# Optimization experiments

Hardware: AMD Instinct MI355X
Metric: run time of the kernel (lower is better)

Reference implementation:

```python
import jax, jax.numpy as jnp
import numpy as np

B, T, E, H, W = 2, 1024, 1024, 8, 31
D = 2 * W + 1  # head dim must equal 2*window_size+1 for the rel-pos broadcast


def _ln(x, w, b):
    mu = jnp.mean(x, axis=-1, keepdims=True)
    var = jnp.mean(jnp.square(x - mu), axis=-1, keepdims=True)
    return (x - mu) * jax.lax.rsqrt(var + 1e-5) * w + b


def setup_inputs() -> dict:
    key = jax.random.key(0)
    k = jax.random.split(key, 8)
    s = 0.02
    return {
        "x": jax.random.normal(k[0], (B, T, E // 2), jnp.float32),
        "ln1_w": jnp.ones(E, jnp.float32), "ln1_b": jnp.zeros(E, jnp.float32),
        "qkv_w": jax.random.normal(k[1], (3 * H * D, E), jnp.float32) * s,
        "qkv_b": jnp.zeros(3 * H * D, jnp.float32),
        "rel_pos": jax.random.normal(k[2], (D, D), jnp.float32) * s,
        "proj_w": jax.random.normal(k[3], (E, H * D), jnp.float32) * s,
        "proj_b": jnp.zeros(E, jnp.float32),
        "ln2_w": jnp.ones(E, jnp.float32), "ln2_b": jnp.zeros(E, jnp.float32),
        "fc_w": jax.random.normal(k[4], (4 * E, E), jnp.float32) * s,
        "fc_b": jnp.zeros(4 * E, jnp.float32),
        "cproj_w": jax.random.normal(k[5], (E, 4 * E), jnp.float32) * s,
        "cproj_b": jnp.zeros(E, jnp.float32),
    }


def reference(x, ln1_w, ln1_b, qkv_w, qkv_b, rel_pos, proj_w, proj_b,
              ln2_w, ln2_b, fc_w, fc_b, cproj_w, cproj_b):
    # --- RotaryEmbedding: angle = x * inv_freq; out = cat(sin, cos) -> [B,T,E]
    dim = 2 * x.shape[-1]
    inv_freq = 1.0 / 10000.0 ** (jnp.arange(0, dim, 2, dtype=jnp.float32) / dim)
    ang = x * inv_freq
    xr = jnp.concatenate([jnp.sin(ang), jnp.cos(ang)], axis=-1)  # [B,T,E]

    # --- custom windowed attention on ln_1(xr)
    h = _ln(xr, ln1_w, ln1_b)
    qkv = h @ qkv_w.T + qkv_b                       # [B,T,3*H*D]
    q, k, v = jnp.split(qkv, 3, axis=-1)

    def heads(t):
        return t.reshape(B, T, H, D).transpose(0, 2, 1, 3)  # [B,H,T,D]

    q, k, v = heads(q), heads(k), heads(v)
    # per-token q-outer-k scores (einsum '...bd,...bv->...bdv'): [B,H,T,D,D]
    scores = jnp.einsum('bhtd,bhtv->bhtdv', q, k)
    # rel-pos bias: Embedding lookup at offsets -W..W (negative indices wrap)
    bias = rel_pos[jnp.arange(-W, W + 1) % D]       # [D, D] == [2W+1, d_model]
    attn = jax.nn.softmax(scores + bias, axis=-2)   # softmax over non-canonical axis
    out = jnp.einsum('bhtdv,bhtv->bhtd', attn, v)   # apply per-token attn matrix to v
    out = out.transpose(0, 2, 1, 3).reshape(B, T, H * D)
    xa = xr + out @ proj_w.T + proj_b               # residual

    # --- MLP
    h2 = _ln(xa, ln2_w, ln2_b)
    m = jax.nn.gelu(h2 @ fc_w.T + fc_b, approximate=False) @ cproj_w.T + cproj_b
    return xa + m
```

## Files before the change

kernel.cpp:

```cpp
#include <hip/hip_runtime.h>
#include <hip/hip_bf16.h>


typedef __bf16 bf16;
typedef bf16 bf16x8 __attribute__((ext_vector_type(8)));
typedef bf16 bf16x4 __attribute__((ext_vector_type(4)));
typedef bf16 bf16x2 __attribute__((ext_vector_type(2)));
typedef float f32x4 __attribute__((ext_vector_type(4)));

__global__ __launch_bounds__(256) void rotary_ln_kernel(
    const float* __restrict__ x, const float* __restrict__ w,
    const float* __restrict__ b, float* __restrict__ xr, bf16* __restrict__ Y)
{
    const int row = blockIdx.x;
    const int tid = threadIdx.x;
    float2 xv = *(const float2*)(x + (size_t)row * 512 + tid * 2);
    float i0 = exp2f(-(float)(2*tid)     * 0.025952563241307518f);
    float i1 = exp2f(-(float)(2*tid + 1) * 0.025952563241307518f);
    float a0 = xv.x * i0, a1 = xv.y * i1;
    float s0 = sinf(a0), s1 = sinf(a1);
    float c0 = cosf(a0), c1 = cosf(a1);
    *(float2*)(xr + (size_t)row * 1024 + tid*2)       = make_float2(s0, s1);
    *(float2*)(xr + (size_t)row * 1024 + 512 + tid*2) = make_float2(c0, c1);
    float s  = s0 + s1 + c0 + c1;
    float ss = s0*s0 + s1*s1 + c0*c0 + c1*c1;
    #pragma unroll
    for (int off = 32; off > 0; off >>= 1) {
        s  += __shfl_down(s, off);
        ss += __shfl_down(ss, off);
    }
    __shared__ float rs[4], rss[4];
    int wave = tid >> 6, lane = tid & 63;
    if (lane == 0) { rs[wave] = s; rss[wave] = ss; }
    __syncthreads();
    s  = rs[0] + rs[1] + rs[2] + rs[3];
    ss = rss[0] + rss[1] + rss[2] + rss[3];
    float mu   = s * (1.f / 1024.f);
    float var  = ss * (1.f / 1024.f) - mu * mu;
    float rstd = rsqrtf(var + 1e-5f);
    float2 w0 = *(const float2*)(w + tid*2);
    float2 b0 = *(const float2*)(b + tid*2);
    float2 w1 = *(const float2*)(w + 512 + tid*2);
    float2 b1 = *(const float2*)(b + 512 + tid*2);
    bf16x2 y0, y1;
    y0[0] = (bf16)((s0 - mu) * rstd * w0.x + b0.x);
    y0[1] = (bf16)((s1 - mu) * rstd * w0.y + b0.y);
    y1[0] = (bf16)((c0 - mu) * rstd * w1.x + b1.x);
    y1[1] = (bf16)((c1 - mu) * rstd * w1.y + b1.y);
    *(bf16x2*)(Y + (size_t)row * 1024 + tid*2)       = y0;
    *(bf16x2*)(Y + (size_t)row * 1024 + 512 + tid*2) = y1;
}

__global__ __launch_bounds__(256) void ln_bf16_kernel(
    const float* __restrict__ X, const float* __restrict__ w,
    const float* __restrict__ b, bf16* __restrict__ Y)
{
    int row = blockIdx.x;
    const float4* xp = (const float4*)(X + (size_t)row * 1024);
    float4 xv = xp[threadIdx.x];
    float s  = xv.x + xv.y + xv.z + xv.w;
    float ss = xv.x*xv.x + xv.y*xv.y + xv.z*xv.z + xv.w*xv.w;
    #pragma unroll
    for (int off = 32; off > 0; off >>= 1) {
        s  += __shfl_down(s, off);
        ss += __shfl_down(ss, off);
    }
    __shared__ float rs[4], rss[4];
    int wave = threadIdx.x >> 6, lane = threadIdx.x & 63;
    if (lane == 0) { rs[wave] = s; rss[wave] = ss; }
    __syncthreads();
    s  = rs[0] + rs[1] + rs[2] + rs[3];
    ss = rss[0] + rss[1] + rss[2] + rss[3];
    float mu  = s * (1.f / 1024.f);
    float var = ss * (1.f / 1024.f) - mu * mu;
    float rstd = rsqrtf(var + 1e-5f);
    float4 wv = ((const float4*)w)[threadIdx.x];
    float4 bv = ((const float4*)b)[threadIdx.x];
    bf16 y[4];
    y[0] = (bf16)((xv.x - mu) * rstd * wv.x + bv.x);
    y[1] = (bf16)((xv.y - mu) * rstd * wv.y + bv.y);
    y[2] = (bf16)((xv.z - mu) * rstd * wv.z + bv.z);
    y[3] = (bf16)((xv.w - mu) * rstd * wv.w + bv.w);
    *(uint2*)(Y + (size_t)row * 1024 + threadIdx.x * 4) = *(uint2*)y;
}

__device__ __forceinline__ void conv_chunk(
    const float* __restrict__ src, bf16* __restrict__ dst,
    int ci, int N, int K, int Kp)
{
    int kpc = Kp >> 3;
    int r  = ci / kpc;
    int kc = (ci - r * kpc) << 3;
    bf16x8 o;
    if (r < N && kc < K) {
        float4 f0 = *(const float4*)(src + (size_t)r * K + kc);
        float4 f1 = *(const float4*)(src + (size_t)r * K + kc + 4);
        o[0]=(bf16)f0.x; o[1]=(bf16)f0.y; o[2]=(bf16)f0.z; o[3]=(bf16)f0.w;
        o[4]=(bf16)f1.x; o[5]=(bf16)f1.y; o[6]=(bf16)f1.z; o[7]=(bf16)f1.w;
    } else {
        #pragma unroll
        for (int j = 0; j < 8; ++j) o[j] = (bf16)0.f;
    }
    *(bf16x8*)(dst + (size_t)r * Kp + kc) = o;
}

__global__ __launch_bounds__(256) void conv_all_kernel(
    const float* __restrict__ qkv_w, const float* __restrict__ proj_w,
    const float* __restrict__ fc_w,  const float* __restrict__ cproj_w,
    const float* __restrict__ qkv_b,
    bf16* __restrict__ wqkv, bf16* __restrict__ wproj,
    bf16* __restrict__ wfc,  bf16* __restrict__ wcproj,
    float* __restrict__ qkvb_p)
{
    if (blockIdx.x == 5120) {
        for (int i = threadIdx.x; i < 1536; i += 256)
            qkvb_p[i] = (i < 1512) ? qkv_b[i] : 0.f;
        return;
    }
    int idx = blockIdx.x * 256 + threadIdx.x;
    if      (idx < 196608)  conv_chunk(qkv_w,   wqkv,   idx,          1512, 1024, 1024);
    else if (idx < 262144)  conv_chunk(proj_w,  wproj,  idx - 196608, 1024,  504,  512);
    else if (idx < 786432)  conv_chunk(fc_w,    wfc,    idx - 262144, 4096, 1024, 1024);
    else                    conv_chunk(cproj_w, wcproj, idx - 786432, 1024, 4096, 4096);
}

__device__ __forceinline__ float gelu_exact(float v)
{
    return 0.5f * v * (1.f + erff(v * 0.70710678118654752f));
}

template<int EPI>
__global__ __launch_bounds__(256, 4) void gemm6_kernel(
    const bf16* __restrict__ A, const bf16* __restrict__ Wt,
    const float* __restrict__ bias,
    float* Cf, bf16* Cb, int N, int Kp, int ksplit)
{
    __shared__ __align__(16) char lds[2][12288];

    const int tid  = threadIdx.x;
    const int w    = tid >> 6;
    const int lane = tid & 63;

    const int gx = gridDim.x, gy = gridDim.y;
    const int nwg = gx * gy * gridDim.z;
    const int chunk = nwg >> 3;
    int id = (blockIdx.z * gy + blockIdx.y) * gx + blockIdx.x;
    int sw = (id & 7) * chunk + (id >> 3);
    const int bx = sw % gx;
    const int t2 = sw / gx;
    const int by = t2 % gy;
    const int bz = t2 / gy;

    const int row0 = by * 64;
    const int col0 = bx * 128;
    const int wr = (w >> 1) * 32;
    const int wc = (w & 1) * 64;
    const int rl = lane & 15;
    const int kb16 = (lane >> 4) * 16;

    const size_t strideBy = (size_t)Kp * 2;
    const size_t kz = (size_t)bz * ksplit * 2;
    const char* Abase = (const char*)A  + (size_t)row0 * strideBy + kz;
    const char* Wbase = (const char*)Wt + (size_t)col0 * strideBy + kz;

    const size_t srcA0 = (size_t)(tid >> 2) * strideBy + (tid & 3) * 16;
    size_t srcB[2];
    #pragma unroll
    for (int i = 0; i < 2; ++i) {
        int o = (i * 256 + tid) * 16;
        srcB[i] = (size_t)(o >> 6) * strideBy + (o & 63);
    }

    f32x4 acc[2][4] = {};

    auto STAGE = [&](int buf, int kt) {
        const char* ab = Abase + (size_t)kt * 64;
        const char* wb = Wbase + (size_t)kt * 64;
        __builtin_amdgcn_global_load_lds(
            (const __attribute__((address_space(1))) void*)(ab + srcA0),
            (__attribute__((address_space(3))) void*)(&lds[buf][0] + tid * 16),
            16, 0, 0);
        #pragma unroll
        for (int i = 0; i < 2; ++i)
            __builtin_amdgcn_global_load_lds(
                (const __attribute__((address_space(1))) void*)(wb + srcB[i]),
                (__attribute__((address_space(3))) void*)(&lds[buf][4096] + (i*256 + tid)*16),
                16, 0, 0);
    };

    const int niter = ksplit >> 5;
    STAGE(0, 0);
    __syncthreads();
    for (int kt = 0; kt < niter; ++kt) {
        if (kt + 1 < niter)
            STAGE((kt + 1) & 1, kt + 1);
        const char* base = lds[kt & 1];
        bf16x8 af[2], bfr[4];
        #pragma unroll
        for (int mi = 0; mi < 2; ++mi)
            af[mi] = *(const bf16x8*)(base + ((wr + mi*16 + rl) << 6) + kb16);
        #pragma unroll
        for (int nj = 0; nj < 4; ++nj)
            bfr[nj] = *(const bf16x8*)(base + 4096 + ((wc + nj*16 + rl) << 6) + kb16);
        __builtin_amdgcn_s_setprio(1);
        #pragma unroll
        for (int mi = 0; mi < 2; ++mi)
            #pragma unroll
            for (int nj = 0; nj < 4; ++nj)
                acc[mi][nj] = __builtin_amdgcn_mfma_f32_16x16x32_bf16(
                    af[mi], bfr[nj], acc[mi][nj], 0, 0, 0);
        __builtin_amdgcn_s_setprio(0);
        __syncthreads();
    }

    const int rq = (lane >> 4) * 4;
    bf16* Cbz = Cb;
    if (EPI == 3) Cbz += (size_t)bz * 2048 * N;
    #pragma unroll
    for (int mi = 0; mi < 2; ++mi) {
        #pragma unroll
        for (int rj = 0; rj < 4; ++rj) {
            int row = row0 + wr + mi*16 + rq + rj;
            #pragma unroll
            for (int nj = 0; nj < 4; ++nj) {
                int col = col0 + wc + nj*16 + rl;
                float c = acc[mi][nj][rj];
                if (EPI != 3) c += bias[col];
                size_t off = (size_t)row * N + col;
                if (EPI == 0)      Cb[off]  = (bf16)c;
                else if (EPI == 1) Cb[off]  = (bf16)gelu_exact(c);
                else               Cbz[off] = (bf16)c;
            }
        }
    }
}

template<int P>
__global__ __launch_bounds__(256) void reduce_kernel(
    const bf16* __restrict__ parts, const float* __restrict__ bias,
    const float* R, float* out)
{
    int row = blockIdx.x;
    int c = threadIdx.x * 4;
    size_t off = (size_t)row * 1024 + c;
    float4 bv = *(const float4*)(bias + c);
    float4 o = *(const float4*)(R + off);
    o.x += bv.x; o.y += bv.y; o.z += bv.z; o.w += bv.w;
    #pragma unroll
    for (int p = 0; p < P; ++p) {
        bf16x4 v = *(const bf16x4*)(parts + (size_t)p * 2048 * 1024 + off);
        o.x += (float)v[0]; o.y += (float)v[1];
        o.z += (float)v[2]; o.w += (float)v[3];
    }
    *(float4*)(out + off) = o;
}

__global__ __launch_bounds__(256) void attn_kernel(
    const bf16* __restrict__ qkv, const float* __restrict__ rel_pos,
    bf16* __restrict__ outp)
{
    __shared__ float sbias[64*65];
    __shared__ float kmw[4][3][64];
    for (int i = threadIdx.x; i < 63*63; i += 256) {
        int d = i / 63, v = i - d*63;
        sbias[d*65 + v] = rel_pos[((d + 32) % 63) * 63 + v];
    }
    __syncthreads();
    const int wave = threadIdx.x >> 6;
    const int lane = threadIdx.x & 63;
    const int tk  = blockIdx.x * 4 + wave;
    const int row = tk >> 3;
    const int h   = tk & 7;
    const bf16* base = qkv + (size_t)row * 1536 + h * 63;
    float q_own = 0.f, k_own = 0.f, v_own = 0.f;
    if (lane < 63) {
        q_own = (float)base[lane];
        k_own = (float)base[504 + lane];
        v_own = (float)base[1008 + lane];
    }
    float m = -1e30f;
    for (int d = 0; d < 63; ++d) {
        float qd = __shfl(q_own, d);
        m = fmaxf(m, fmaf(qd, k_own, sbias[d*65 + lane]));
    }
    float Z = 0.f;
    for (int d = 0; d < 63; ++d) {
        float qd = __shfl(q_own, d);
        Z += __expf(fmaf(qd, k_own, sbias[d*65 + lane]) - m);
    }
    kmw[wave][0][lane] = k_own;
    kmw[wave][1][lane] = m;
    kmw[wave][2][lane] = v_own / Z;
    float acc = 0.f;
    for (int v = 0; v < 63; ++v) {
        float s = fmaf(q_own, kmw[wave][0][v], sbias[lane*65 + v]) - kmw[wave][1][v];
        acc += __expf(s) * kmw[wave][2][v];
    }
    if (lane < 63)
        outp[(size_t)row * 512 + h*63 + lane] = (bf16)acc;
    if (h == 7 && lane == 63) {
        #pragma unroll
        for (int j = 0; j < 8; ++j)
            outp[(size_t)row * 512 + 504 + j] = (bf16)0.f;
    }
}

extern "C" void kernel_launch(void* const* d_in, const int* in_sizes, int n_in,
                              void* d_out, int out_size, void* d_ws, size_t ws_size,
                              hipStream_t stream)
{
    const float* x       = (const float*)d_in[0];
    const float* ln1_w   = (const float*)d_in[1];
    const float* ln1_b   = (const float*)d_in[2];
    const float* qkv_w   = (const float*)d_in[3];
    const float* qkv_b   = (const float*)d_in[4];
    const float* rel_pos = (const float*)d_in[5];
    const float* proj_w  = (const float*)d_in[6];
    const float* proj_b  = (const float*)d_in[7];
    const float* ln2_w   = (const float*)d_in[8];
    const float* ln2_b   = (const float*)d_in[9];
    const float* fc_w    = (const float*)d_in[10];
    const float* fc_b    = (const float*)d_in[11];
    const float* cproj_w = (const float*)d_in[12];
    const float* cproj_b = (const float*)d_in[13];
    float* out = (float*)d_out;

    char* p = (char*)d_ws;
    float* xr      = (float*)p;            p += (size_t)2048*1024*4;
    bf16*  h_bf    = (bf16*)p;             p += (size_t)2048*1024*2;
    bf16*  wqkv    = (bf16*)p;             p += (size_t)1536*1024*2;
    bf16*  wproj   = (bf16*)p;             p += (size_t)1024*512*2;
    bf16*  wfc     = (bf16*)p;             p += (size_t)4096*1024*2;
    bf16*  wcproj  = (bf16*)p;             p += (size_t)1024*4096*2;
    float* qkvb_p  = (float*)p;            p += 8192;
    bf16*  attn_bf = (bf16*)p;             p += (size_t)2048*512*2;
    bf16*  qkvb    = (bf16*)p;
    bf16*  fc_act  = (bf16*)p;
    bf16*  proj_part = qkvb;
    bf16*  cp_part = (bf16*)d_ws;

    conv_all_kernel<<<5121, 256, 0, stream>>>(qkv_w, proj_w, fc_w, cproj_w, qkv_b,
                                              wqkv, wproj, wfc, wcproj, qkvb_p);
    rotary_ln_kernel<<<2048, 256, 0, stream>>>(x, ln1_w, ln1_b, xr, h_bf);
    gemm6_kernel<0><<<dim3(12,32,1), 256, 0, stream>>>(h_bf, wqkv, qkvb_p,
                                                       nullptr, qkvb, 1536, 1024, 1024);
    attn_kernel<<<4096, 256, 0, stream>>>(qkvb, rel_pos, attn_bf);
    gemm6_kernel<3><<<dim3(8,32,2), 256, 0, stream>>>(attn_bf, wproj, nullptr,
                                                      nullptr, proj_part, 1024, 512, 256);
    reduce_kernel<2><<<2048, 256, 0, stream>>>(proj_part, proj_b, xr, out);
    ln_bf16_kernel<<<2048, 256, 0, stream>>>(out, ln2_w, ln2_b, h_bf);
    gemm6_kernel<1><<<dim3(32,32,1), 256, 0, stream>>>(h_bf, wfc, fc_b,
                                                       nullptr, fc_act, 4096, 1024, 1024);
    gemm6_kernel<3><<<dim3(8,32,4), 256, 0, stream>>>(fc_act, wcproj, nullptr,
                                                      nullptr, cp_part, 1024, 4096, 1024);
    reduce_kernel<4><<<2048, 256, 0, stream>>>(cp_part, cproj_b, out, out);
}
```

Before: 152.9 us.

## Fuse proj reduction with LN2 and rewrite attention with readlane and swizzled bias

Merges the split-K reduction of the projection GEMM with the second layernorm into one kernel, removing a launch and a full re-read of the residual. Rewrites the per-token attention kernel to drop the max pass, broadcasting q/k/w via readlane and reading bias from XOR-swizzled LDS tables (row and transposed) with vectorized loads. Padding entries are set to -1e30 so lane 63 contributes nothing. Skipping the max subtraction risks exp overflow if scores grow large. Also cleans up the GEMM signature.

New measurement: 149.9 us. 2.0% less time.

```diff
diff --git a/kernel.cpp b/kernel.cpp
--- a/kernel.cpp
+++ b/kernel.cpp
@@ -7,6 +7,11 @@
 typedef bf16 bf16x4 __attribute__((ext_vector_type(4)));
 typedef bf16 bf16x2 __attribute__((ext_vector_type(2)));
 typedef float f32x4 __attribute__((ext_vector_type(4)));
+
+__device__ __forceinline__ float rdlane(float x, int l)
+{
+    return __int_as_float(__builtin_amdgcn_readlane(__float_as_int(x), l));
+}
 
 __global__ __launch_bounds__(256) void rotary_ln_kernel(
     const float* __restrict__ x, const float* __restrict__ w,
@@ -51,39 +56,6 @@
     *(bf16x2*)(Y + (size_t)row * 1024 + 512 + tid*2) = y1;
 }
 
-__global__ __launch_bounds__(256) void ln_bf16_kernel(
-    const float* __restrict__ X, const float* __restrict__ w,
-    const float* __restrict__ b, bf16* __restrict__ Y)
-{
-    int row = blockIdx.x;
-    const float4* xp = (const float4*)(X + (size_t)row * 1024);
-    float4 xv = xp[threadIdx.x];
-    float s  = xv.x + xv.y + xv.z + xv.w;
-    float ss = xv.x*xv.x + xv.y*xv.y + xv.z*xv.z + xv.w*xv.w;
-    #pragma unroll
-    for (int off = 32; off > 0; off >>= 1) {
-        s  += __shfl_down(s, off);
-        ss += __shfl_down(ss, off);
-    }
-    __shared__ float rs[4], rss[4];
-    int wave = threadIdx.x >> 6, lane = threadIdx.x & 63;
-    if (lane == 0) { rs[wave] = s; rss[wave] = ss; }
-    __syncthreads();
-    s  = rs[0] + rs[1] + rs[2] + rs[3];
-    ss = rss[0] + rss[1] + rss[2] + rss[3];
-    float mu  = s * (1.f / 1024.f);
-    float var = ss * (1.f / 1024.f) - mu * mu;
-    float rstd = rsqrtf(var + 1e-5f);
-    float4 wv = ((const float4*)w)[threadIdx.x];
-    float4 bv = ((const float4*)b)[threadIdx.x];
-    bf16 y[4];
-    y[0] = (bf16)((xv.x - mu) * rstd * wv.x + bv.x);
-    y[1] = (bf16)((xv.y - mu) * rstd * wv.y + bv.y);
-    y[2] = (bf16)((xv.z - mu) * rstd * wv.z + bv.z);
-    y[3] = (bf16)((xv.w - mu) * rstd * wv.w + bv.w);
-    *(uint2*)(Y + (size_t)row * 1024 + threadIdx.x * 4) = *(uint2*)y;
-}
-
 __device__ __forceinline__ void conv_chunk(
     const float* __restrict__ src, bf16* __restrict__ dst,
     int ci, int N, int K, int Kp)
@@ -124,6 +96,12 @@
     else                    conv_chunk(cproj_w, wcproj, idx - 786432, 1024, 4096, 4096);
 }
 
+__device__ __forceinline__ void gload16(const char* src, char* ldsdst)
+{
+    __builtin_amdgcn_global_load_lds(
+        (const __attribute__((address_space(1))) void*)src,
+        (__attribute__((address_space(3))) void*)ldsdst, 16, 0, 0);
+}
 __device__ __forceinline__ float gelu_exact(float v)
 {
     return 0.5f * v * (1.f + erff(v * 0.70710678118654752f));
@@ -132,8 +110,8 @@
 template<int EPI>
 __global__ __launch_bounds__(256, 4) void gemm6_kernel(
     const bf16* __restrict__ A, const bf16* __restrict__ Wt,
-    const float* __restrict__ bias,
-    float* Cf, bf16* Cb, int N, int Kp, int ksplit)
+    const float* __restrict__ bias, bf16* __restrict__ Cb,
+    int N, int Kp, int ksplit)
 {
     __shared__ __align__(16) char lds[2][12288];
 
@@ -176,16 +154,10 @@
     auto STAGE = [&](int buf, int kt) {
         const char* ab = Abase + (size_t)kt * 64;
         const char* wb = Wbase + (size_t)kt * 64;
-        __builtin_amdgcn_global_load_lds(
-            (const __attribute__((address_space(1))) void*)(ab + srcA0),
-            (__attribute__((address_space(3))) void*)(&lds[buf][0] + tid * 16),
-            16, 0, 0);
+        gload16(ab + srcA0, &lds[buf][0] + tid * 16);
         #pragma unroll
         for (int i = 0; i < 2; ++i)
-            __builtin_amdgcn_global_load_lds(
-                (const __attribute__((address_space(1))) void*)(wb + srcB[i]),
-                (__attribute__((address_space(3))) void*)(&lds[buf][4096] + (i*256 + tid)*16),
-                16, 0, 0);
+            gload16(wb + srcB[i], &lds[buf][4096] + (i * 256 + tid) * 16);
     };
 
     const int niter = ksplit >> 5;
@@ -225,10 +197,9 @@
             for (int nj = 0; nj < 4; ++nj) {
                 int col = col0 + wc + nj*16 + rl;
                 float c = acc[mi][nj][rj];
-                if (EPI != 3) c += bias[col];
                 size_t off = (size_t)row * N + col;
-                if (EPI == 0)      Cb[off]  = (bf16)c;
-                else if (EPI == 1) Cb[off]  = (bf16)gelu_exact(c);
+                if (EPI == 0)      Cbz[off] = (bf16)(c + bias[col]);
+                else if (EPI == 1) Cbz[off] = (bf16)gelu_exact(c + bias[col]);
                 else               Cbz[off] = (bf16)c;
             }
         }
@@ -255,17 +226,66 @@
     *(float4*)(out + off) = o;
 }
 
-__global__ __launch_bounds__(256) void attn_kernel(
+__global__ __launch_bounds__(256) void reduceln_kernel(
+    const bf16* __restrict__ parts, const float* __restrict__ bias,
+    const float* __restrict__ R, const float* __restrict__ lnw,
+    const float* __restrict__ lnb, float* __restrict__ out,
+    bf16* __restrict__ Y)
+{
+    int row = blockIdx.x;
+    int c = threadIdx.x * 4;
+    size_t off = (size_t)row * 1024 + c;
+    float4 bv = *(const float4*)(bias + c);
+    float4 o  = *(const float4*)(R + off);
+    o.x += bv.x; o.y += bv.y; o.z += bv.z; o.w += bv.w;
+    #pragma unroll
+    for (int p = 0; p < 2; ++p) {
+        bf16x4 v = *(const bf16x4*)(parts + (size_t)p * 2048 * 1024 + off);
+        o.x += (float)v[0]; o.y += (float)v[1];
+        o.z += (float)v[2]; o.w += (float)v[3];
+    }
+    *(float4*)(out + off) = o;
+    float s  = o.x + o.y + o.z + o.w;
+    float ss = o.x*o.x + o.y*o.y + o.z*o.z + o.w*o.w;
+    #pragma unroll
+    for (int of = 32; of > 0; of >>= 1) {
+        s  += __shfl_down(s, of);
+        ss += __shfl_down(ss, of);
+    }
+    __shared__ float rs[4], rss[4];
+    int wave = threadIdx.x >> 6, lane = threadIdx.x & 63;
+    if (lane == 0) { rs[wave] = s; rss[wave] = ss; }
+    __syncthreads();
+    s  = rs[0] + rs[1] + rs[2] + rs[3];
+    ss = rss[0] + rss[1] + rss[2] + rss[3];
+    float mu  = s * (1.f / 1024.f);
+    float var = ss * (1.f / 1024.f) - mu * mu;
+    float rstd = rsqrtf(var + 1e-5f);
+    float4 wv = *(const float4*)(lnw + c);
+    float4 lb = *(const float4*)(lnb + c);
+    bf16 y[4];
+    y[0] = (bf16)((o.x - mu) * rstd * wv.x + lb.x);
+    y[1] = (bf16)((o.y - mu) * rstd * wv.y + lb.y);
+    y[2] = (bf16)((o.z - mu) * rstd * wv.z + lb.z);
+    y[3] = (bf16)((o.w - mu) * rstd * wv.w + lb.w);
+    *(uint2*)(Y + (size_t)row * 1024 + c) = *(uint2*)y;
+}
+
+__global__ __launch_bounds__(256) void attn2_kernel(
     const bf16* __restrict__ qkv, const float* __restrict__ rel_pos,
     bf16* __restrict__ outp)
 {
-    __shared__ float sbias[64*65];
-    __shared__ float kmw[4][3][64];
-    for (int i = threadIdx.x; i < 63*63; i += 256) {
-        int d = i / 63, v = i - d*63;
-        sbias[d*65 + v] = rel_pos[((d + 32) % 63) * 63 + v];
+    __shared__ float bR[4096];
+    __shared__ float bT[4096];
+    for (int i = threadIdx.x; i < 4096; i += 256) {
+        int d = i >> 6, v = i & 63;
+        float val = (d < 63 && v < 63)
+                  ? rel_pos[((d + 32) % 63) * 63 + v] : -1e30f;
+        bR[(d << 6) + (((v >> 2) ^ (d & 15)) << 2) + (v & 3)] = val;
+        bT[(v << 6) + (((d >> 2) ^ (v & 15)) << 2) + (d & 3)] = val;
     }
     __syncthreads();
+
     const int wave = threadIdx.x >> 6;
     const int lane = threadIdx.x & 63;
     const int tk  = blockIdx.x * 4 + wave;
@@ -278,24 +298,37 @@
         k_own = (float)base[504 + lane];
         v_own = (float)base[1008 + lane];
     }
-    float m = -1e30f;
-    for (int d = 0; d < 63; ++d) {
-        float qd = __shfl(q_own, d);
-        m = fmaxf(m, fmaf(qd, k_own, sbias[d*65 + lane]));
-    }
-    float Z = 0.f;
-    for (int d = 0; d < 63; ++d) {
-        float qd = __shfl(q_own, d);
-        Z += __expf(fmaf(qd, k_own, sbias[d*65 + lane]) - m);
-    }
-    kmw[wave][0][lane] = k_own;
-    kmw[wave][1][lane] = m;
-    kmw[wave][2][lane] = v_own / Z;
-    float acc = 0.f;
-    for (int v = 0; v < 63; ++v) {
-        float s = fmaf(q_own, kmw[wave][0][v], sbias[lane*65 + v]) - kmw[wave][1][v];
-        acc += __expf(s) * kmw[wave][2][v];
-    }
+
+    const float* myT = bT + (lane << 6);
+    const int sw = lane & 15;
+    float z0 = 0.f, z1 = 0.f, z2 = 0.f, z3 = 0.f;
+    #pragma unroll
+    for (int g = 0; g < 16; ++g) {
+        f32x4 bb = *(const f32x4*)(myT + ((g ^ sw) << 2));
+        z0 += __expf(fmaf(rdlane(q_own, 4*g + 0), k_own, bb[0]));
+        z1 += __expf(fmaf(rdlane(q_own, 4*g + 1), k_own, bb[1]));
+        z2 += __expf(fmaf(rdlane(q_own, 4*g + 2), k_own, bb[2]));
+        z3 += __expf(fmaf(rdlane(q_own, 4*g + 3), k_own, bb[3]));
+    }
+    float Z = (z0 + z1) + (z2 + z3);
+    float w_own = (lane < 63) ? v_own / Z : 0.f;
+
+    const float* myR = bR + (lane << 6);
+    float a0 = 0.f, a1 = 0.f, a2 = 0.f, a3 = 0.f;
+    #pragma unroll
+    for (int g = 0; g < 16; ++g) {
+        f32x4 bb = *(const f32x4*)(myR + ((g ^ sw) << 2));
+        a0 = fmaf(__expf(fmaf(q_own, rdlane(k_own, 4*g + 0), bb[0])),
+                  rdlane(w_own, 4*g + 0), a0);
+        a1 = fmaf(__expf(fmaf(q_own, rdlane(k_own, 4*g + 1), bb[1])),
+                  rdlane(w_own, 4*g + 1), a1);
+        a2 = fmaf(__expf(fmaf(q_own, rdlane(k_own, 4*g + 2), bb[2])),
+                  rdlane(w_own, 4*g + 2), a2);
+        a3 = fmaf(__expf(fmaf(q_own, rdlane(k_own, 4*g + 3), bb[3])),
+                  rdlane(w_own, 4*g + 3), a3);
+    }
+    float acc = (a0 + a1) + (a2 + a3);
+
     if (lane < 63)
         outp[(size_t)row * 512 + h*63 + lane] = (bf16)acc;
     if (h == 7 && lane == 63) {
@@ -343,15 +376,15 @@
                                               wqkv, wproj, wfc, wcproj, qkvb_p);
     rotary_ln_kernel<<<2048, 256, 0, stream>>>(x, ln1_w, ln1_b, xr, h_bf);
     gemm6_kernel<0><<<dim3(12,32,1), 256, 0, stream>>>(h_bf, wqkv, qkvb_p,
-                                                       nullptr, qkvb, 1536, 1024, 1024);
-    attn_kernel<<<4096, 256, 0, stream>>>(qkvb, rel_pos, attn_bf);
+                                                       qkvb, 1536, 1024, 1024);
+    attn2_kernel<<<4096, 256, 0, stream>>>(qkvb, rel_pos, attn_bf);
     gemm6_kernel<3><<<dim3(8,32,2), 256, 0, stream>>>(attn_bf, wproj, nullptr,
-                                                      nullptr, proj_part, 1024, 512, 256);
-    reduce_kernel<2><<<2048, 256, 0, stream>>>(proj_part, proj_b, xr, out);
-    ln_bf16_kernel<<<2048, 256, 0, stream>>>(out, ln2_w, ln2_b, h_bf);
+                                                      proj_part, 1024, 512, 256);
+    reduceln_kernel<<<2048, 256, 0, stream>>>(proj_part, proj_b, xr,
+                                              ln2_w, ln2_b, out, h_bf);
     gemm6_kernel<1><<<dim3(32,32,1), 256, 0, stream>>>(h_bf, wfc, fc_b,
-                                                       nullptr, fc_act, 4096, 1024, 1024);
+                                                       fc_act, 4096, 1024, 1024);
     gemm6_kernel<3><<<dim3(8,32,4), 256, 0, stream>>>(fc_act, wcproj, nullptr,
-                                                      nullptr, cp_part, 1024, 4096, 1024);
+                                                      cp_part, 1024, 4096, 1024);
     reduce_kernel<4><<<2048, 256, 0, stream>>>(cp_part, cproj_b, out, out);
 }
```
